# Kernel tuning notes

Hardware: AMD Instinct MI355X
Metric: run time of the kernel (lower is better)

Reference implementation:

```python
import jax, jax.numpy as jnp
import numpy as np

N = 8192
D = 512

def _row_normalize(m):
    # row-normalize; rows summing to 0 get inverse 0 (inf -> 0 in original)
    rs = m.sum(axis=1, keepdims=True)
    inv = jnp.where(rs == 0, 0.0, 1.0 / rs)
    return m * inv

def setup_inputs() -> dict:
    key = jax.random.key(0)
    k1, k2 = jax.random.split(key)
    qf = jax.random.normal(k1, (N, D), dtype=jnp.float32)
    gf = jax.random.normal(k2, (N, D), dtype=jnp.float32)
    return {"qf": qf, "gf": gf}

def reference(qf, gf):
    # feature = row-normalized squared difference  [N, D]
    feature = _row_normalize((qf - gf) ** 2)
    # adj[i, j] = ||feature_i - feature_j||^2, via GEMM expansion
    sq = jnp.sum(feature * feature, axis=-1)                  # [N]
    adj = sq[:, None] + sq[None, :] - 2.0 * (feature @ feature.T)  # [N, N]
    # symmetrize: elementwise max(adj, adj.T) (equivalent to the masked mix)
    adj = jnp.maximum(adj, adj.T)
    # add identity and row-normalize
    adj = adj + jnp.eye(N, dtype=adj.dtype)
    adj = _row_normalize(adj)
    return adj, feature
```

## Files before the change

kernel.cpp:

```cpp
#include <hip/hip_runtime.h>
#include <hip/hip_bf16.h>

#define N 8192
#define D 512

typedef __attribute__((ext_vector_type(8))) short short8;
typedef __attribute__((ext_vector_type(4))) float f32x4;

__device__ __forceinline__ float block_reduce_256(float v, float* red) {
    #pragma unroll
    for (int o = 1; o < 64; o <<= 1) v += __shfl_xor(v, o, 64);
    int w = threadIdx.x >> 6;
    if ((threadIdx.x & 63) == 0) red[w] = v;
    __syncthreads();
    float tot = red[0] + red[1] + red[2] + red[3];
    __syncthreads();
    return tot;
}

__global__ void feature_kernel(const float* __restrict__ qf, const float* __restrict__ gf,
                               float* __restrict__ feat, __hip_bfloat16* __restrict__ featb,
                               float* __restrict__ sq) {
    __shared__ float red[4];
    int row = blockIdx.x, t = threadIdx.x;
    const float2* q2 = (const float2*)(qf + (size_t)row * D);
    const float2* g2 = (const float2*)(gf + (size_t)row * D);
    float2 qv = q2[t], gv = g2[t];
    float a = qv.x - gv.x, b = qv.y - gv.y;
    float va = a * a, vb = b * b;
    float rs = block_reduce_256(va + vb, red);
    float inv = (rs == 0.0f) ? 0.0f : 1.0f / rs;
    float fa = va * inv, fb = vb * inv;
    ((float2*)(feat + (size_t)row * D))[t] = make_float2(fa, fb);
    __hip_bfloat162 h;
    h.x = __float2bfloat16(fa);
    h.y = __float2bfloat16(fb);
    ((__hip_bfloat162*)(featb + (size_t)row * D))[t] = h;
    float tot = block_reduce_256(fa * fa + fb * fb, red);
    if (t == 0) sq[row] = tot;
}

__global__ void colsum_partial_kernel(const float* __restrict__ feat, float* __restrict__ partial) {
    int b = blockIdx.x, t = threadIdx.x;
    const float* fp = feat + (size_t)b * 128 * D;
    float a0 = 0.f, a1 = 0.f;
    for (int r = 0; r < 128; ++r) {
        a0 += fp[r * D + t];
        a1 += fp[r * D + t + 256];
    }
    partial[b * D + t] = a0;
    partial[b * D + t + 256] = a1;
}

__global__ void finalize_kernel(const float* __restrict__ partial, const float* __restrict__ sq,
                                float* __restrict__ cvec, float* __restrict__ Sval) {
    __shared__ float red[4];
    int t = threadIdx.x;
    if (blockIdx.x == 0) {
        float a0 = 0.f, a1 = 0.f;
        for (int b = 0; b < 64; ++b) {
            a0 += partial[b * D + t];
            a1 += partial[b * D + t + 256];
        }
        cvec[t] = a0;
        cvec[t + 256] = a1;
    } else {
        float s = 0.f;
        for (int k = 0; k < N / 256; ++k) s += sq[t + 256 * k];
        float tot = block_reduce_256(s, red);
        if (t == 0) Sval[0] = tot;
    }
}

__global__ void rowinv_kernel(const float* __restrict__ feat, const float* __restrict__ sq,
                              const float* __restrict__ cvec, const float* __restrict__ Sval,
                              float* __restrict__ rowinv) {
    __shared__ float red[4];
    int row = blockIdx.x, t = threadIdx.x;
    float2 f = ((const float2*)(feat + (size_t)row * D))[t];
    float2 c = ((const float2*)cvec)[t];
    float dot = block_reduce_256(f.x * c.x + f.y * c.y, red);
    if (t == 0) {
        float rs = (float)N * sq[row] + Sval[0] - 2.0f * dot + 1.0f;
        rowinv[row] = (rs == 0.0f) ? 0.0f : 1.0f / rs;
    }
}

__global__ __launch_bounds__(256, 3) void adj_gemm_sym_kernel(const __hip_bfloat16* __restrict__ featb,
                                                              const float* __restrict__ sq,
                                                              const float* __restrict__ rowinv,
                                                              float* __restrict__ out) {
    __shared__ __align__(16) char lds[16384];
    int wg = blockIdx.x;
    int id = (wg & 7) * 260 + (wg >> 3);
    int r = (int)((129.0f - sqrtf(16641.0f - 8.0f * (float)id)) * 0.5f);
    if (r > 63) r = 63;
    while (r > 0 && (r * (129 - r)) / 2 > id) --r;
    while (((r + 1) * (128 - r)) / 2 <= id) ++r;
    int by = r;
    int bx = r + (id - (r * (129 - r)) / 2);
    int rowBase = by * 128, colBase = bx * 128;

    int t = threadIdx.x, lane = t & 63, w = t >> 6;
    int wr = w >> 1, wc = w & 1, g = lane >> 4;

    f32x4 acc[4][4];
    #pragma unroll
    for (int m = 0; m < 4; ++m)
        #pragma unroll
        for (int n = 0; n < 4; ++n) acc[m][n] = (f32x4){0.f, 0.f, 0.f, 0.f};

    int r0 = t >> 2, cc = t & 3;
    int s0 = (r0 >> 1) & 3;
    int woff = r0 * 64 + ((cc ^ s0) * 16);
    const __hip_bfloat16* gA0 = featb + (size_t)(rowBase + r0) * D + cc * 8;
    const __hip_bfloat16* gB0 = featb + (size_t)(colBase + r0) * D + cc * 8;
    char* ldsA = lds;
    char* ldsB = lds + 8192;

    for (int ks = 0; ks < D / 32; ++ks) {
        int k0 = ks * 32;
        short8 vA0 = *(const short8*)(gA0 + k0);
        short8 vA1 = *(const short8*)(gA0 + 64 * D + k0);
        short8 vB0 = *(const short8*)(gB0 + k0);
        short8 vB1 = *(const short8*)(gB0 + 64 * D + k0);
        *(short8*)(ldsA + woff)        = vA0;
        *(short8*)(ldsA + woff + 4096) = vA1;
        *(short8*)(ldsB + woff)        = vB0;
        *(short8*)(ldsB + woff + 4096) = vB1;
        __syncthreads();

        short8 afrag[4], bfrag[4];
        #pragma unroll
        for (int m = 0; m < 4; ++m) {
            int rr = wr * 64 + m * 16 + (lane & 15);
            int c16 = (lane >> 4) ^ ((rr >> 1) & 3);
            afrag[m] = *(const short8*)(ldsA + rr * 64 + c16 * 16);
        }
        #pragma unroll
        for (int n = 0; n < 4; ++n) {
            int rr = wc * 64 + n * 16 + (lane & 15);
            int c16 = (lane >> 4) ^ ((rr >> 1) & 3);
            bfrag[n] = *(const short8*)(ldsB + rr * 64 + c16 * 16);
        }
        #pragma unroll
        for (int m = 0; m < 4; ++m)
            #pragma unroll
            for (int n = 0; n < 4; ++n)
                acc[m][n] = __builtin_amdgcn_mfma_f32_16x16x32_bf16(afrag[m], bfrag[n], acc[m][n], 0, 0, 0);
        __syncthreads();
    }

    float sqj[4], rj4[4];
    int jcol[4];
    #pragma unroll
    for (int n = 0; n < 4; ++n) {
        jcol[n] = colBase + wc * 64 + n * 16 + (lane & 15);
        sqj[n] = sq[jcol[n]];
        rj4[n] = rowinv[jcol[n]];
    }
    int offdiag = (by != bx);
    #pragma unroll
    for (int m = 0; m < 4; ++m) {
        int i0 = rowBase + wr * 64 + m * 16 + g * 4;
        float si0 = sq[i0], si1 = sq[i0 + 1], si2 = sq[i0 + 2], si3 = sq[i0 + 3];
        float ri0 = rowinv[i0], ri1 = rowinv[i0 + 1], ri2 = rowinv[i0 + 2], ri3 = rowinv[i0 + 3];
        #pragma unroll
        for (int n = 0; n < 4; ++n) {
            int j = jcol[n];
            float pre0 = si0 + sqj[n] - 2.0f * acc[m][n][0] + (i0 == j ? 1.0f : 0.0f);
            float pre1 = si1 + sqj[n] - 2.0f * acc[m][n][1] + (i0 + 1 == j ? 1.0f : 0.0f);
            float pre2 = si2 + sqj[n] - 2.0f * acc[m][n][2] + (i0 + 2 == j ? 1.0f : 0.0f);
            float pre3 = si3 + sqj[n] - 2.0f * acc[m][n][3] + (i0 + 3 == j ? 1.0f : 0.0f);
            out[(size_t)(i0 + 0) * N + j] = pre0 * ri0;
            out[(size_t)(i0 + 1) * N + j] = pre1 * ri1;
            out[(size_t)(i0 + 2) * N + j] = pre2 * ri2;
            out[(size_t)(i0 + 3) * N + j] = pre3 * ri3;
            if (offdiag) {
                f32x4 v;
                v[0] = pre0 * rj4[n];
                v[1] = pre1 * rj4[n];
                v[2] = pre2 * rj4[n];
                v[3] = pre3 * rj4[n];
                *(f32x4*)&out[(size_t)j * N + i0] = v;
            }
        }
    }
}

extern "C" void kernel_launch(void* const* d_in, const int* in_sizes, int n_in,
                              void* d_out, int out_size, void* d_ws, size_t ws_size,
                              hipStream_t stream) {
    const float* qf = (const float*)d_in[0];
    const float* gf = (const float*)d_in[1];
    float* out = (float*)d_out;
    float* feat = out + (size_t)N * N;

    char* wsb = (char*)d_ws;
    __hip_bfloat16* featb = (__hip_bfloat16*)wsb;
    float* sq      = (float*)(wsb + 8388608);
    float* partial = (float*)(wsb + 8388608 + 32768);
    float* cvec    = (float*)(wsb + 8388608 + 32768 + 131072);
    float* Sval    = (float*)(wsb + 8388608 + 32768 + 131072 + 2048);
    float* rowinv  = (float*)(wsb + 8388608 + 32768 + 131072 + 2048 + 64);

    feature_kernel<<<N, 256, 0, stream>>>(qf, gf, feat, featb, sq);
    colsum_partial_kernel<<<64, 256, 0, stream>>>(feat, partial);
    finalize_kernel<<<2, 256, 0, stream>>>(partial, sq, cvec, Sval);
    rowinv_kernel<<<N, 256, 0, stream>>>(feat, sq, cvec, Sval, rowinv);
    adj_gemm_sym_kernel<<<2080, 256, 0, stream>>>(featb, sq, rowinv, out);
}
```

Measured before the change: 124.9 us.

## Use 256x256 tiles with 1024 threads and async double-buffered global-to-LDS loads

Raises the symmetric GEMM tile from 128x128 to 256x256 and uses 16 waves per workgroup, cutting the grid to 528 upper-triangular tiles. Operand loads now go straight from global memory to LDS through global_load_lds into two buffers, so the next K slice is prefetched while MFMAs run on the current one, with explicit waitcnt and barriers plus raised wave priority during the MFMA block. This aims to improve operand reuse and hide load latency, at the cost of 64KB LDS per block and fewer, larger blocks. That may leave some compute units idle and makes the diagonal-tile waste larger.

```diff
diff --git a/kernel.cpp b/kernel.cpp
--- a/kernel.cpp
+++ b/kernel.cpp
@@ -86,23 +86,23 @@
     }
 }
 
-__global__ __launch_bounds__(256, 3) void adj_gemm_sym_kernel(const __hip_bfloat16* __restrict__ featb,
-                                                              const float* __restrict__ sq,
-                                                              const float* __restrict__ rowinv,
-                                                              float* __restrict__ out) {
-    __shared__ __align__(16) char lds[16384];
+__global__ __launch_bounds__(1024, 4) void adj_gemm_sym_kernel(const __hip_bfloat16* __restrict__ featb,
+                                                               const float* __restrict__ sq,
+                                                               const float* __restrict__ rowinv,
+                                                               float* __restrict__ out) {
+    __shared__ __align__(16) char lds[65536];
     int wg = blockIdx.x;
-    int id = (wg & 7) * 260 + (wg >> 3);
-    int r = (int)((129.0f - sqrtf(16641.0f - 8.0f * (float)id)) * 0.5f);
-    if (r > 63) r = 63;
-    while (r > 0 && (r * (129 - r)) / 2 > id) --r;
-    while (((r + 1) * (128 - r)) / 2 <= id) ++r;
+    int id = (wg & 7) * 66 + (wg >> 3);
+    int r = (int)((65.0f - sqrtf(4225.0f - 8.0f * (float)id)) * 0.5f);
+    if (r > 31) r = 31;
+    while (r > 0 && (r * (65 - r)) / 2 > id) --r;
+    while (((r + 1) * (64 - r)) / 2 <= id) ++r;
     int by = r;
-    int bx = r + (id - (r * (129 - r)) / 2);
-    int rowBase = by * 128, colBase = bx * 128;
+    int bx = r + (id - (r * (65 - r)) / 2);
+    int rowBase = by * 256, colBase = bx * 256;
 
     int t = threadIdx.x, lane = t & 63, w = t >> 6;
-    int wr = w >> 1, wc = w & 1, g = lane >> 4;
+    int wrow = w >> 2, wcol = w & 3, g = lane >> 4;
 
     f32x4 acc[4][4];
     #pragma unroll
@@ -110,59 +110,68 @@
         #pragma unroll
         for (int n = 0; n < 4; ++n) acc[m][n] = (f32x4){0.f, 0.f, 0.f, 0.f};
 
-    int r0 = t >> 2, cc = t & 3;
-    int s0 = (r0 >> 1) & 3;
-    int woff = r0 * 64 + ((cc ^ s0) * 16);
-    const __hip_bfloat16* gA0 = featb + (size_t)(rowBase + r0) * D + cc * 8;
-    const __hip_bfloat16* gB0 = featb + (size_t)(colBase + r0) * D + cc * 8;
-    char* ldsA = lds;
-    char* ldsB = lds + 8192;
-
-    for (int ks = 0; ks < D / 32; ++ks) {
-        int k0 = ks * 32;
-        short8 vA0 = *(const short8*)(gA0 + k0);
-        short8 vA1 = *(const short8*)(gA0 + 64 * D + k0);
-        short8 vB0 = *(const short8*)(gB0 + k0);
-        short8 vB1 = *(const short8*)(gB0 + 64 * D + k0);
-        *(short8*)(ldsA + woff)        = vA0;
-        *(short8*)(ldsA + woff + 4096) = vA1;
-        *(short8*)(ldsB + woff)        = vB0;
-        *(short8*)(ldsB + woff + 4096) = vB1;
-        __syncthreads();
-
-        short8 afrag[4], bfrag[4];
-        #pragma unroll
-        for (int m = 0; m < 4; ++m) {
-            int rr = wr * 64 + m * 16 + (lane & 15);
-            int c16 = (lane >> 4) ^ ((rr >> 1) & 3);
-            afrag[m] = *(const short8*)(ldsA + rr * 64 + c16 * 16);
+    int srow = t >> 2;
+    int cg = (t & 3) ^ ((srow >> 1) & 3);
+    const __hip_bfloat16* gA = featb + (size_t)(rowBase + srow) * D + cg * 8;
+    const __hip_bfloat16* gB = featb + (size_t)(colBase + srow) * D + cg * 8;
+    int dstw = w * 1024;
+
+#define STAGE(buf, kb) do { \
+    __builtin_amdgcn_global_load_lds((const void*)(gA + (kb)), (void*)(lds + (buf) * 16384 + dstw), 16, 0, 0); \
+    __builtin_amdgcn_global_load_lds((const void*)(gB + (kb)), (void*)(lds + 32768 + (buf) * 16384 + dstw), 16, 0, 0); \
+} while (0)
+
+    STAGE(0, 0);
+
+    int arow = wrow * 64 + (lane & 15);
+    int brow = wcol * 64 + (lane & 15);
+    int caA = (g ^ ((arow >> 1) & 3)) << 4;
+    int caB = (g ^ ((brow >> 1) & 3)) << 4;
+
+    for (int kt = 0; kt < 16; ++kt) {
+        int cur = kt & 1;
+        if (kt < 15) STAGE(cur ^ 1, (kt + 1) * 32);
+        __builtin_amdgcn_sched_barrier(0);
+        if (kt < 15) asm volatile("s_waitcnt vmcnt(2)" ::: "memory");
+        else         asm volatile("s_waitcnt vmcnt(0)" ::: "memory");
+        __builtin_amdgcn_s_barrier();
+        __builtin_amdgcn_sched_barrier(0);
+
+        const char* pA = lds + cur * 16384;
+        const char* pB = lds + 32768 + cur * 16384;
+        short8 af[4];
+        #pragma unroll
+        for (int m = 0; m < 4; ++m)
+            af[m] = *(const short8*)(pA + (arow + 16 * m) * 64 + caA);
+        __builtin_amdgcn_s_setprio(1);
+        #pragma unroll
+        for (int n = 0; n < 4; ++n) {
+            short8 bf = *(const short8*)(pB + (brow + 16 * n) * 64 + caB);
+            #pragma unroll
+            for (int m = 0; m < 4; ++m)
+                acc[m][n] = __builtin_amdgcn_mfma_f32_16x16x32_bf16(af[m], bf, acc[m][n], 0, 0, 0);
         }
-        #pragma unroll
-        for (int n = 0; n < 4; ++n) {
-            int rr = wc * 64 + n * 16 + (lane & 15);
-            int c16 = (lane >> 4) ^ ((rr >> 1) & 3);
-            bfrag[n] = *(const short8*)(ldsB + rr * 64 + c16 * 16);
-        }
-        #pragma unroll
-        for (int m = 0; m < 4; ++m)
-            #pragma unroll
-            for (int n = 0; n < 4; ++n)
-                acc[m][n] = __builtin_amdgcn_mfma_f32_16x16x32_bf16(afrag[m], bfrag[n], acc[m][n], 0, 0, 0);
-        __syncthreads();
-    }
+        __builtin_amdgcn_s_setprio(0);
+
+        asm volatile("s_waitcnt lgkmcnt(0)" ::: "memory");
+        __builtin_amdgcn_sched_barrier(0);
+        __builtin_amdgcn_s_barrier();
+        __builtin_amdgcn_sched_barrier(0);
+    }
+#undef STAGE
 
     float sqj[4], rj4[4];
     int jcol[4];
     #pragma unroll
     for (int n = 0; n < 4; ++n) {
-        jcol[n] = colBase + wc * 64 + n * 16 + (lane & 15);
+        jcol[n] = colBase + wcol * 64 + n * 16 + (lane & 15);
         sqj[n] = sq[jcol[n]];
         rj4[n] = rowinv[jcol[n]];
     }
     int offdiag = (by != bx);
     #pragma unroll
     for (int m = 0; m < 4; ++m) {
-        int i0 = rowBase + wr * 64 + m * 16 + g * 4;
+        int i0 = rowBase + wrow * 64 + m * 16 + g * 4;
         float si0 = sq[i0], si1 = sq[i0 + 1], si2 = sq[i0 + 2], si3 = sq[i0 + 3];
         float ri0 = rowinv[i0], ri1 = rowinv[i0 + 1], ri2 = rowinv[i0 + 2], ri3 = rowinv[i0 + 3];
         #pragma unroll
@@ -208,5 +217,5 @@
     colsum_partial_kernel<<<64, 256, 0, stream>>>(feat, partial);
     finalize_kernel<<<2, 256, 0, stream>>>(partial, sq, cvec, Sval);
     rowinv_kernel<<<N, 256, 0, stream>>>(feat, sq, cvec, Sval, rowinv);
-    adj_gemm_sym_kernel<<<2080, 256, 0, stream>>>(featb, sq, rowinv, out);
-}
+    adj_gemm_sym_kernel<<<528, 1024, 0, stream>>>(featb, sq, rowinv, out);
+}
```

New measurement: 136.9 us. +9.6%, slower.
